# Kernel tuning notes

Hardware: AMD Instinct MI355X
Metric: run time of the kernel (lower is better)

Reference implementation:

```python
import jax, jax.numpy as jnp
import numpy as np

B, NR, NP, E, F, EIN, H, OUT = 2, 16384, 65536, 262144, 128, 4, 16, 4
EPS = 1e-6

def _mlp(x, W1, b1, W2, b2):
    return jax.nn.swish(x @ W1 + b1) @ W2 + b2

def _cond_norm(x, tau, C1, c1, C2, c2):
    # conditioned LayerNorm: scale/shift computed from tau by a shallow MLP
    h = jax.nn.swish(tau @ C1 + c1)               # [B, H]
    scale, shift = jnp.split(h @ C2 + c2, 2, -1)  # [B, F] each
    mu = jnp.mean(x, -1, keepdims=True)
    var = jnp.var(x, -1, keepdims=True)
    xn = (x - mu) * jax.lax.rsqrt(var + EPS)
    return xn * (1.0 + scale[:, None, :]) + shift[:, None, :]

def _segment_mean(feat, recv, num_segments):
    seg = lambda f, r: jax.ops.segment_sum(f, r, num_segments=num_segments)
    s = jax.vmap(seg)(feat, recv)
    cnt = jax.vmap(seg)(jnp.ones(recv.shape, feat.dtype), recv)
    return s / jnp.maximum(cnt, 1.0)[..., None]

def setup_inputs():
    key = jax.random.key(0)
    ks = iter(jax.random.split(key, 48))
    dense = lambda i, o: jax.random.normal(next(ks), (i, o), jnp.float32) / np.sqrt(i)
    inp = {}
    inp['rnode_features'] = jax.random.normal(next(ks), (B, NR, F), jnp.float32)
    inp['pnode_features'] = jax.random.normal(next(ks), (B, NP, F), jnp.float32)
    inp['edge_features'] = jax.random.normal(next(ks), (B, E, EIN), jnp.float32)
    inp['tau'] = jax.random.uniform(next(ks), (B, 1), jnp.float32)
    # edge embedding MLP + cond norm
    inp['We1'], inp['We2'] = dense(EIN, F), dense(F, F)
    inp['be1'], inp['be2'] = jnp.zeros((F,)), jnp.zeros((F,))
    inp['Ce1'], inp['Ce2'] = dense(1, H), dense(H, 2 * F)
    inp['ce1'], inp['ce2'] = jnp.zeros((H,)), jnp.zeros((2 * F,))
    # edge update MLP + cond norm
    inp['Wu1'], inp['Wu2'] = dense(3 * F, F), dense(F, F)
    inp['bu1'], inp['bu2'] = jnp.zeros((F,)), jnp.zeros((F,))
    inp['Cu1'], inp['Cu2'] = dense(1, H), dense(H, 2 * F)
    inp['cu1'], inp['cu2'] = jnp.zeros((H,)), jnp.zeros((2 * F,))
    # pnode update MLP + cond norm
    inp['Wp1'], inp['Wp2'] = dense(2 * F, F), dense(F, F)
    inp['bp1'], inp['bp2'] = jnp.zeros((F,)), jnp.zeros((F,))
    inp['Cp1'], inp['Cp2'] = dense(1, H), dense(H, 2 * F)
    inp['cp1'], inp['cp2'] = jnp.zeros((H,)), jnp.zeros((2 * F,))
    # rnode update MLP + cond norm
    inp['Wr1'], inp['Wr2'] = dense(F, F), dense(F, F)
    inp['br1'], inp['br2'] = jnp.zeros((F,)), jnp.zeros((F,))
    inp['Cr1'], inp['Cr2'] = dense(1, H), dense(H, 2 * F)
    inp['cr1'], inp['cr2'] = jnp.zeros((H,)), jnp.zeros((2 * F,))
    # pnode output MLP (no norm)
    inp['Wo1'], inp['Wo2'] = dense(F, F), dense(F, OUT)
    inp['bo1'], inp['bo2'] = jnp.zeros((F,)), jnp.zeros((OUT,))
    inp['senders'] = jax.random.randint(next(ks), (B, E), 0, NR, jnp.int32)
    inp['receivers'] = jax.random.randint(next(ks), (B, E), 0, NP, jnp.int32)
    return inp

def reference(rnode_features, pnode_features, edge_features, tau,
              We1, be1, We2, be2, Ce1, ce1, Ce2, ce2,
              Wu1, bu1, Wu2, bu2, Cu1, cu1, Cu2, cu2,
              Wp1, bp1, Wp2, bp2, Cp1, cp1, Cp2, cp2,
              Wr1, br1, Wr2, br2, Cr1, cr1, Cr2, cr2,
              Wo1, bo1, Wo2, bo2, senders, receivers):
    # 1) embed raw r2p edge features to latent size (embed_edges=True)
    e = _cond_norm(_mlp(edge_features, We1, be1, We2, be2), tau, Ce1, ce1, Ce2, ce2)
    # 2) one message-passing step: edge update from gathered sender/receiver feats
    sf = jnp.take_along_axis(rnode_features, senders[..., None], axis=1)    # [B,E,F]
    rf = jnp.take_along_axis(pnode_features, receivers[..., None], axis=1)  # [B,E,F]
    e = e + _cond_norm(_mlp(jnp.concatenate([e, sf, rf], -1), Wu1, bu1, Wu2, bu2),
                       tau, Cu1, cu1, Cu2, cu2)
    # 3) pnode update with segment_mean aggregation, residual
    agg = _segment_mean(e, receivers, NP)                                   # [B,NP,F]
    p = pnode_features + _cond_norm(
        _mlp(jnp.concatenate([pnode_features, agg], -1), Wp1, bp1, Wp2, bp2),
        tau, Cp1, cp1, Cp2, cp2)
    # 4) rnode update (no incoming edges; structurally present but unused by output)
    r = rnode_features + _cond_norm(_mlp(rnode_features, Wr1, br1, Wr2, br2),
                                    tau, Cr1, cr1, Cr2, cr2)
    del r
    # 5) output MLP on pnodes (node_output_size=dict(pnodes=num_outputs))
    return _mlp(p, Wo1, bo1, Wo2, bo2)
```

## Files before the change

### kernel.cpp

```cpp
#include <hip/hip_runtime.h>

constexpr int cB  = 2;
constexpr int cNR = 16384;
constexpr int cNP = 65536;
constexpr int cE  = 262144;
constexpr int cF  = 128;
constexpr int cEB = cE / 64;
constexpr int SP  = 136;
constexpr int EFP = 40;

typedef unsigned short u16;
using f32x4 = __attribute__((ext_vector_type(4))) float;
using s8v   = __attribute__((ext_vector_type(8))) short;

constexpr int G8_We2 = 0, G8_Wu1 = 16, G8_Wu2 = 64, G8_Wp1 = 80, G8_Wp2 = 112, G8_Wo1 = 128;
constexpr int G8_TOT = 144;
constexpr int SWZ_N = G8_TOT * 128 + 256 + 512;
constexpr int WB_WE1 = (G8_TOT * 128 + 256) * 8;

constexpr size_t WS_CNT  = 0;
constexpr size_t WS_POS  = WS_CNT + (size_t)cB * cNP;
constexpr size_t WS_BSUM = WS_POS + (size_t)cB * cNP;
constexpr size_t WS_SS   = WS_BSUM + 512;
constexpr size_t WS_WB   = WS_SS + 3 * cB * 256;
constexpr size_t WS_RB   = WS_WB + (size_t)SWZ_N * 4;
constexpr size_t WS_PB   = WS_RB + (size_t)cB * cNR * cF / 2;
constexpr size_t WS_EL   = WS_PB + (size_t)cB * cNP * cF / 2;
constexpr size_t WS_EB   = WS_EL + (size_t)cB * cE;

__device__ __forceinline__ float bf2f(u16 u) {
  union { unsigned int i; float f; } v; v.i = ((unsigned int)u) << 16; return v.f;
}
__device__ __forceinline__ u16 f2bf(float f) {
  union { float f; unsigned int i; } v; v.f = f;
  unsigned int x = v.i;
  return (u16)((x + 0x7fffu + ((x >> 16) & 1u)) >> 16);
}
__device__ __forceinline__ u16 f2bf_fast(float f) {
  return (u16)((__float_as_uint(f) + 0x8000u) >> 16);
}
__device__ __forceinline__ unsigned pack2(float a, float b) {
  return __builtin_amdgcn_perm(__float_as_uint(b) + 0x8000u,
                               __float_as_uint(a) + 0x8000u, 0x07060302u);
}
__device__ __forceinline__ float swishf(float x) {
  return x * __builtin_amdgcn_rcpf(1.0f + __expf(-x));
}

template <int CTRL>
__device__ __forceinline__ float dpp_add(float x) {
  int xi = __float_as_int(x);
  int r = __builtin_amdgcn_update_dpp(xi, xi, CTRL, 0xf, 0xf, false);
  return x + __int_as_float(r);
}

__device__ __forceinline__ void gload4_lds(const u16* gsrc, u16* lds) {
  __builtin_amdgcn_global_load_lds(
      (const __attribute__((address_space(1))) void*)gsrc,
      (__attribute__((address_space(3))) void*)lds, 4, 0, 0);
}

__device__ __forceinline__ void kloop128s(const u16* act, const u16* __restrict__ wbg,
                                          f32x4 (&acc)[4][2], int cw, int l16, int quad) {
  s8v bf[4][2];
#pragma unroll
  for (int k0 = 0; k0 < 4; ++k0)
#pragma unroll
    for (int ci = 0; ci < 2; ++ci)
      bf[k0][ci] = *(const s8v*)(wbg + ((size_t)(k0 * 4 + quad) * 128 + cw + ci * 16 + l16) * 8);
#pragma unroll
  for (int k0 = 0; k0 < 4; ++k0) {
    s8v af[4];
#pragma unroll
    for (int ri = 0; ri < 4; ++ri)
      af[ri] = *(const s8v*)(act + (size_t)(ri * 16 + l16) * SP + k0 * 32 + quad * 8);
#pragma unroll
    for (int ri = 0; ri < 4; ++ri)
#pragma unroll
      for (int ci = 0; ci < 2; ++ci)
        acc[ri][ci] = __builtin_amdgcn_mfma_f32_16x16x32_bf16(af[ri], bf[k0][ci], acc[ri][ci], 0, 0, 0);
  }
}

__device__ __forceinline__ void init_acc_s(f32x4 (&acc)[4][2], const float* __restrict__ bias,
                                           int cw, int l16) {
#pragma unroll
  for (int ci = 0; ci < 2; ++ci) {
    float bv = bias[cw + ci * 16 + l16];
#pragma unroll
    for (int ri = 0; ri < 4; ++ri) acc[ri][ci] = (f32x4){bv, bv, bv, bv};
  }
}

__device__ __forceinline__ void cond_norm_s(f32x4 (&acc)[4][2], float* red, float* musig,
                                            const float* __restrict__ ssp,
                                            int cw, int l16, int quad, int wv, int t) {
  __syncthreads();
#pragma unroll
  for (int ri = 0; ri < 4; ++ri)
#pragma unroll
    for (int reg = 0; reg < 4; ++reg) {
      float v0 = acc[ri][0][reg], v1 = acc[ri][1][reg];
      float s = v0 + v1;
      float q = v0 * v0 + v1 * v1;
      s = dpp_add<0x128>(s); q = dpp_add<0x128>(q);
      s = dpp_add<0x124>(s); q = dpp_add<0x124>(q);
      s = dpp_add<0x122>(s); q = dpp_add<0x122>(q);
      s = dpp_add<0x121>(s); q = dpp_add<0x121>(q);
      if (l16 == 0) {
        int row = ri * 16 + quad * 4 + reg;
        red[row * 8 + wv * 2]     = s;
        red[row * 8 + wv * 2 + 1] = q;
      }
    }
  __syncthreads();
  if (t < 64) {
    float sum = red[t * 8 + 0] + red[t * 8 + 2] + red[t * 8 + 4] + red[t * 8 + 6];
    float sq  = red[t * 8 + 1] + red[t * 8 + 3] + red[t * 8 + 5] + red[t * 8 + 7];
    float mu  = sum * (1.0f / 128.0f);
    float var = fmaxf(sq * (1.0f / 128.0f) - mu * mu, 0.0f);
    musig[t * 2]     = mu;
    musig[t * 2 + 1] = __builtin_amdgcn_rsqf(var + 1e-6f);
  }
  __syncthreads();
  float scl[2], shf[2];
#pragma unroll
  for (int ci = 0; ci < 2; ++ci) {
    int col = cw + ci * 16 + l16;
    scl[ci] = 1.0f + ssp[col];
    shf[ci] = ssp[128 + col];
  }
#pragma unroll
  for (int ri = 0; ri < 4; ++ri)
#pragma unroll
    for (int reg = 0; reg < 4; ++reg) {
      int row = ri * 16 + quad * 4 + reg;
      float mu = musig[row * 2], is = musig[row * 2 + 1];
#pragma unroll
      for (int ci = 0; ci < 2; ++ci)
        acc[ri][ci][reg] = (acc[ri][ci][reg] - mu) * is * scl[ci] + shf[ci];
    }
}

template <bool DOSWISH>
__device__ __forceinline__ void store_s(u16* buf, const f32x4 (&acc)[4][2],
                                        int cw, int l16, int quad) {
#pragma unroll
  for (int ri = 0; ri < 4; ++ri)
#pragma unroll
    for (int reg = 0; reg < 4; ++reg) {
      int row = ri * 16 + quad * 4 + reg;
#pragma unroll
      for (int ci = 0; ci < 2; ++ci) {
        float v = acc[ri][ci][reg];
        if (DOSWISH) v = swishf(v);
        buf[(size_t)row * SP + cw + ci * 16 + l16] = f2bf_fast(v);
      }
    }
}

__global__ void zero_kernel(float4* __restrict__ p, int n4) {
  int i = blockIdx.x * 256 + threadIdx.x;
  if (i < n4) p[i] = make_float4(0.f, 0.f, 0.f, 0.f);
}

__global__ void cvtn_kernel(const float* __restrict__ src, u16* __restrict__ dst, int n2) {
  int i = blockIdx.x * 256 + threadIdx.x;
  if (i >= n2) return;
  float2 v = ((const float2*)src)[i];
  ((unsigned*)dst)[i] = pack2(v.x, v.y);
}

__global__ void hist_kernel(const int* __restrict__ receivers, int* __restrict__ cntI) {
  int i = blockIdx.x * 256 + threadIdx.x;
  if (i >= cB * cE) return;
  int b = i / cE;
  int r = min(max(receivers[i], 0), cNP - 1);
  atomicAdd(&cntI[(size_t)b * cNP + r], 1);
}

__global__ void scanA_kernel(const int* __restrict__ cntI, int* __restrict__ bsum) {
  __shared__ int red[256];
  int g = blockIdx.x, t = threadIdx.x;
  red[t] = cntI[g * 256 + t];
  __syncthreads();
  for (int s = 128; s > 0; s >>= 1) {
    if (t < s) red[t] += red[t + s];
    __syncthreads();
  }
  if (t == 0) bsum[g] = red[0];
}

__global__ void scanB_kernel(int* __restrict__ bsum) {
  __shared__ int s0[512], s1[512];
  int t = threadIdx.x;
  int v0 = bsum[t];
  s0[t] = v0;
  __syncthreads();
  int* src = s0; int* dst = s1;
  for (int s = 1; s < 512; s <<= 1) {
    dst[t] = src[t] + ((t >= s) ? src[t - s] : 0);
    __syncthreads();
    int* tmp = src; src = dst; dst = tmp;
  }
  bsum[t] = src[t] - v0;
}

__global__ void scanC_kernel(const int* __restrict__ cntI, const int* __restrict__ bsum,
                             int* __restrict__ pos) {
  __shared__ int s0[256], s1[256];
  int g = blockIdx.x, t = threadIdx.x;
  int v0 = cntI[g * 256 + t];
  s0[t] = v0;
  __syncthreads();
  int* src = s0; int* dst = s1;
  for (int s = 1; s < 256; s <<= 1) {
    dst[t] = src[t] + ((t >= s) ? src[t - s] : 0);
    __syncthreads();
    int* tmp = src; src = dst; dst = tmp;
  }
  pos[g * 256 + t] = src[t] - v0 + bsum[g];
}

__global__ void fill_kernel(const int* __restrict__ receivers, int* __restrict__ pos,
                            int* __restrict__ elist) {
  int i = blockIdx.x * 256 + threadIdx.x;
  if (i >= cB * cE) return;
  int b = i / cE, e = i - b * cE;
  int r = min(max(receivers[i], 0), cNP - 1);
  int idx = atomicAdd(&pos[(size_t)b * cNP + r], 1);
  elist[idx] = e;
}

struct SwzSrc { const float* p[7]; };

__global__ void swz_kernel(SwzSrc s, const float* __restrict__ Wo2, u16* __restrict__ wb) {
  int t = blockIdx.x * 256 + threadIdx.x;
  if (t >= SWZ_N) return;
  if (t >= G8_TOT * 128 + 256) {
    int idx3 = t - (G8_TOT * 128 + 256);
    int k8 = idx3 >> 7, n = idx3 & 127;
    const float* We1 = s.p[6];
    u16 v[8];
#pragma unroll
    for (int j = 0; j < 8; ++j) {
      int k = k8 * 8 + j;
      v[j] = (k < 4) ? f2bf(We1[(size_t)k * 128 + n]) : (u16)0;
    }
    ((uint4*)wb)[t] = *(uint4*)v;
    return;
  }
  if (t >= G8_TOT * 128) {
    int idx2 = t - G8_TOT * 128;
    int k8 = idx2 >> 4, n = idx2 & 15;
    u16 v[8];
#pragma unroll
    for (int j = 0; j < 8; ++j)
      v[j] = (n < 4) ? f2bf(Wo2[(size_t)(k8 * 8 + j) * 4 + n]) : (u16)0;
    ((uint4*)wb)[G8_TOT * 128 + k8 * 16 + n] = *(uint4*)v;
    return;
  }
  int n = t & 127, g8 = t >> 7;
  int seg, base;
  if (g8 < G8_Wu1)      { seg = 0; base = G8_We2; }
  else if (g8 < G8_Wu2) { seg = 1; base = G8_Wu1; }
  else if (g8 < G8_Wp1) { seg = 2; base = G8_Wu2; }
  else if (g8 < G8_Wp2) { seg = 3; base = G8_Wp1; }
  else if (g8 < G8_Wo1) { seg = 4; base = G8_Wp2; }
  else                  { seg = 5; base = G8_Wo1; }
  const float* W = s.p[seg];
  int k8l = g8 - base;
  u16 v[8];
#pragma unroll
  for (int j = 0; j < 8; ++j) v[j] = f2bf(W[(size_t)(k8l * 8 + j) * 128 + n]);
  ((uint4*)wb)[g8 * 128 + n] = *(uint4*)v;
}

__global__ void cond_kernel(const float* __restrict__ tau,
                            const float* __restrict__ Ce1, const float* __restrict__ ce1,
                            const float* __restrict__ Ce2, const float* __restrict__ ce2,
                            const float* __restrict__ Cu1, const float* __restrict__ cu1,
                            const float* __restrict__ Cu2, const float* __restrict__ cu2,
                            const float* __restrict__ Cp1, const float* __restrict__ cp1,
                            const float* __restrict__ Cp2, const float* __restrict__ cp2,
                            float* __restrict__ ss) {
  int set = blockIdx.x, b = blockIdx.y, j = threadIdx.x;
  const float *C1, *c1, *C2, *c2;
  if (set == 0)      { C1 = Ce1; c1 = ce1; C2 = Ce2; c2 = ce2; }
  else if (set == 1) { C1 = Cu1; c1 = cu1; C2 = Cu2; c2 = cu2; }
  else               { C1 = Cp1; c1 = cp1; C2 = Cp2; c2 = cp2; }
  float tf = tau[b];
  float a = c2[j];
  for (int k = 0; k < 16; ++k) {
    float h = swishf(tf * C1[k] + c1[k]);
    a = fmaf(h, C2[k * 256 + j], a);
  }
  ss[(size_t)set * cB * 256 + (size_t)b * 256 + j] = a;
}

struct EWb { const float *be1, *be2, *bu1, *bu2; };

struct __align__(16) EdgeSmem {
  u16 bufE[64 * SP];
  u16 bufX[64 * SP];
  union {
    u16 ef[64 * EFP];
    struct { float red[512]; float musig[128]; } r;
  } u;
  int sidx[64], ridx[64];
};

__global__ __launch_bounds__(256, 4) void edge_mfma(
    const u16* __restrict__ rnb, const u16* __restrict__ pnb,
    const float* __restrict__ efeat, const int* __restrict__ senders,
    const int* __restrict__ receivers, const int* __restrict__ elist,
    EWb w, const u16* __restrict__ wb,
    const float* __restrict__ ss, u16* __restrict__ ebuf) {
  __shared__ EdgeSmem sm;
  const int t = threadIdx.x, wv = t >> 6, lane = t & 63, l16 = lane & 15, quad = lane >> 4;
  const int cw = wv * 32;
  const int raw = blockIdx.x;
  const int swz = (raw & 7) * (cB * cEB / 8) + (raw >> 3);
  const int b   = swz / cEB;

  if (t < 64) {
    int eid = elist[(size_t)swz * 64 + t];
    size_t ge = (size_t)b * cE + eid;
    sm.sidx[t] = min(max(senders[ge], 0), cNR - 1);
    sm.ridx[t] = min(max(receivers[ge], 0), cNP - 1);
    float4 ef = *(const float4*)(efeat + ge * 4);
    uint4 w0 = { pack2(ef.x, ef.y), pack2(ef.z, ef.w), 0u, 0u };
    uint4 zz = { 0u, 0u, 0u, 0u };
    uint4* rowp = (uint4*)(sm.u.ef + (size_t)t * EFP);
    rowp[0] = w0; rowp[1] = zz; rowp[2] = zz; rowp[3] = zz; rowp[4] = zz;
  }
  __syncthreads();

  f32x4 acc[4][2];

  init_acc_s(acc, w.be1, cw, l16);
  {
    const u16* wbe1 = wb + WB_WE1;
    s8v bf0 = *(const s8v*)(wbe1 + ((size_t)quad * 128 + cw + l16) * 8);
    s8v bf1 = *(const s8v*)(wbe1 + ((size_t)quad * 128 + cw + 16 + l16) * 8);
#pragma unroll
    for (int ri = 0; ri < 4; ++ri) {
      s8v af = *(const s8v*)(sm.u.ef + (size_t)(ri * 16 + l16) * EFP + quad * 8);
      acc[ri][0] = __builtin_amdgcn_mfma_f32_16x16x32_bf16(af, bf0, acc[ri][0], 0, 0, 0);
      acc[ri][1] = __builtin_amdgcn_mfma_f32_16x16x32_bf16(af, bf1, acc[ri][1], 0, 0, 0);
    }
  }
  store_s<true>(sm.bufX, acc, cw, l16, quad);
  __syncthreads();

  init_acc_s(acc, w.be2, cw, l16);
  kloop128s(sm.bufX, wb + (size_t)G8_We2 * 1024, acc, cw, l16, quad);
  cond_norm_s(acc, sm.u.r.red, sm.u.r.musig, ss + (size_t)b * 256, cw, l16, quad, wv, t);
  store_s<false>(sm.bufE, acc, cw, l16, quad);

#pragma unroll
  for (int rr = 0; rr < 16; ++rr) {
    int row = wv * 16 + rr;
    gload4_lds(rnb + ((size_t)b * cNR + sm.sidx[row]) * cF + lane * 2,
               sm.bufX + (size_t)row * SP);
  }
  f32x4 accU[4][2];
  init_acc_s(accU, w.bu1, cw, l16);
  __syncthreads();
  kloop128s(sm.bufX, wb + (size_t)(G8_Wu1 + 16) * 1024, accU, cw, l16, quad);
  __syncthreads();
#pragma unroll
  for (int rr = 0; rr < 16; ++rr) {
    int row = wv * 16 + rr;
    gload4_lds(pnb + ((size_t)b * cNP + sm.ridx[row]) * cF + lane * 2,
               sm.bufX + (size_t)row * SP);
  }
  kloop128s(sm.bufE, wb + (size_t)G8_Wu1 * 1024, accU, cw, l16, quad);
  __syncthreads();
  kloop128s(sm.bufX, wb + (size_t)(G8_Wu1 + 32) * 1024, accU, cw, l16, quad);
  __syncthreads();
  store_s<true>(sm.bufX, accU, cw, l16, quad);
  __syncthreads();

  init_acc_s(acc, w.bu2, cw, l16);
  kloop128s(sm.bufX, wb + (size_t)G8_Wu2 * 1024, acc, cw, l16, quad);
  cond_norm_s(acc, sm.u.r.red, sm.u.r.musig, ss + (size_t)(cB + b) * 256, cw, l16, quad, wv, t);

#pragma unroll
  for (int ri = 0; ri < 4; ++ri)
#pragma unroll
    for (int reg = 0; reg < 4; ++reg) {
      int row = ri * 16 + quad * 4 + reg;
#pragma unroll
      for (int ci = 0; ci < 2; ++ci)
        acc[ri][ci][reg] += bf2f(sm.bufE[(size_t)row * SP + cw + ci * 16 + l16]);
    }
  store_s<false>(sm.bufX, acc, cw, l16, quad);
  __syncthreads();
#pragma unroll
  for (int rr = 0; rr < 16; ++rr) {
    int row = wv * 16 + rr;
    unsigned v = *(const unsigned*)(sm.bufX + (size_t)row * SP + lane * 2);
    ((unsigned*)ebuf)[((size_t)(swz * 64 + row)) * 64 + lane] = v;
  }
}

struct PWb { const float *bp1, *bp2, *bo1, *bo2; };

struct __align__(16) PnodeSmem {
  u16 bufP[64 * SP];
  u16 bufX[64 * SP];
  float red[512];
  float musig[128];
  float cinv[64];
  int startA[64];
  int endA[72];
};

__global__ __launch_bounds__(256, 4) void pnode_mfma(
    const u16* __restrict__ pnb, PWb w, const u16* __restrict__ wb,
    const float* __restrict__ ss, const unsigned* __restrict__ eb32,
    const int* __restrict__ cntI, const int* __restrict__ pos,
    float* __restrict__ out) {
  __shared__ PnodeSmem sm;
  const int t = threadIdx.x, wv = t >> 6, lane = t & 63, l16 = lane & 15, quad = lane >> 4;
  const int cw = wv * 32;
  const int b  = blockIdx.y;
  const int n0 = blockIdx.x * 64;

  if (t < 64) {
    size_t g = (size_t)b * cNP + n0 + t;
    int c  = cntI[g];
    int e_ = pos[g];
    sm.startA[t] = e_ - c;
    sm.endA[t]   = e_;
    sm.cinv[t]   = __builtin_amdgcn_rcpf(fmaxf((float)c, 1.0f));
  } else if (t < 72) {
    sm.endA[t] = 0x7fffffff;
  }
  __syncthreads();

#pragma unroll
  for (int rr = 0; rr < 16; ++rr) {
    int row = wv * 16 + rr;
    unsigned pvu = *(const unsigned*)(pnb + (((size_t)b * cNP + n0 + row) * cF + lane * 2));
    *(unsigned*)(sm.bufP + (size_t)row * SP + lane * 2) = pvu;
  }

  {
    const int nodeLo = wv * 16;
    int cur  = nodeLo;
    int bnd  = sm.endA[cur];
    int s    = sm.startA[nodeLo];
    const int sEnd = sm.endA[nodeLo + 15];
    float a0 = 0.f, a1 = 0.f;
    for (; s < sEnd; s += 8) {
      unsigned v[8];
      int m = sEnd - s;
#pragma unroll
      for (int j = 0; j < 8; ++j)
        if (j < m) v[j] = eb32[(size_t)(s + j) * 64 + lane];
#pragma unroll
      for (int j = 0; j < 8; ++j) {
        if (j < m) {
          while (s + j == bnd) {
            float ci = sm.cinv[cur];
            *(unsigned*)(sm.bufX + (size_t)cur * SP + lane * 2) = pack2(a0 * ci, a1 * ci);
            a0 = a1 = 0.f; ++cur; bnd = sm.endA[cur];
          }
          a0 += bf2f((u16)(v[j] & 0xffffu));
          a1 += bf2f((u16)(v[j] >> 16));
        }
      }
    }
    while (cur < nodeLo + 16) {
      float ci = sm.cinv[cur];
      *(unsigned*)(sm.bufX + (size_t)cur * SP + lane * 2) = pack2(a0 * ci, a1 * ci);
      a0 = a1 = 0.f; ++cur;
    }
  }
  __syncthreads();

  f32x4 acc[4][2];

  init_acc_s(acc, w.bp1, cw, l16);
  kloop128s(sm.bufP, wb + (size_t)G8_Wp1 * 1024, acc, cw, l16, quad);
  kloop128s(sm.bufX, wb + (size_t)(G8_Wp1 + 16) * 1024, acc, cw, l16, quad);
  __syncthreads();
  store_s<true>(sm.bufX, acc, cw, l16, quad);
  __syncthreads();

  init_acc_s(acc, w.bp2, cw, l16);
  kloop128s(sm.bufX, wb + (size_t)G8_Wp2 * 1024, acc, cw, l16, quad);
  cond_norm_s(acc, sm.red, sm.musig, ss + (size_t)(2 * cB + b) * 256, cw, l16, quad, wv, t);
#pragma unroll
  for (int ri = 0; ri < 4; ++ri)
#pragma unroll
    for (int reg = 0; reg < 4; ++reg) {
      int row = ri * 16 + quad * 4 + reg;
#pragma unroll
      for (int ci = 0; ci < 2; ++ci)
        acc[ri][ci][reg] += bf2f(sm.bufP[(size_t)row * SP + cw + ci * 16 + l16]);
    }
  __syncthreads();
  store_s<false>(sm.bufP, acc, cw, l16, quad);
  __syncthreads();

  init_acc_s(acc, w.bo1, cw, l16);
  kloop128s(sm.bufP, wb + (size_t)G8_Wo1 * 1024, acc, cw, l16, quad);
  store_s<true>(sm.bufX, acc, cw, l16, quad);
  __syncthreads();

  {
    const u16* wo2 = wb + (size_t)G8_TOT * 1024;
    float bv = (l16 < 4) ? w.bo2[l16] : 0.0f;
    f32x4 a1 = {bv, bv, bv, bv};
#pragma unroll
    for (int k0 = 0; k0 < 4; ++k0) {
      s8v af = *(const s8v*)(sm.bufX + (size_t)(wv * 16 + l16) * SP + k0 * 32 + quad * 8);
      s8v bf = *(const s8v*)(wo2 + ((size_t)(k0 * 4 + quad) * 16 + l16) * 8);
      a1 = __builtin_amdgcn_mfma_f32_16x16x32_bf16(af, bf, a1, 0, 0, 0);
    }
    if (l16 < 4) {
      size_t obase = (size_t)b * cNP + n0 + wv * 16 + quad * 4;
#pragma unroll
      for (int reg = 0; reg < 4; ++reg)
        out[(obase + reg) * 4 + l16] = a1[reg];
    }
  }
}

extern "C" void kernel_launch(void* const* d_in, const int* in_sizes, int n_in,
                              void* d_out, int out_size, void* d_ws, size_t ws_size,
                              hipStream_t stream) {
  const float* rnode = (const float*)d_in[0];
  const float* pnode = (const float*)d_in[1];
  const float* efeat = (const float*)d_in[2];
  const float* tau   = (const float*)d_in[3];
  const int* senders   = (const int*)d_in[40];
  const int* receivers = (const int*)d_in[41];
  float* ws = (float*)d_ws;
  int* cntI  = (int*)(ws + WS_CNT);
  int* pos   = (int*)(ws + WS_POS);
  int* bsum  = (int*)(ws + WS_BSUM);
  u16* wb    = (u16*)(ws + WS_WB);
  u16* rnb   = (u16*)(ws + WS_RB);
  u16* pnb   = (u16*)(ws + WS_PB);
  int* elist = (int*)(ws + WS_EL);
  u16* ebuf  = (u16*)(ws + WS_EB);

  SwzSrc sw;
  sw.p[0] = (const float*)d_in[5];
  sw.p[1] = (const float*)d_in[12];
  sw.p[2] = (const float*)d_in[13];
  sw.p[3] = (const float*)d_in[20];
  sw.p[4] = (const float*)d_in[21];
  sw.p[5] = (const float*)d_in[36];
  sw.p[6] = (const float*)d_in[4];
  swz_kernel<<<(SWZ_N + 255) / 256, 256, 0, stream>>>(sw, (const float*)d_in[37], wb);

  const int nrn2 = (int)((size_t)cB * cNR * cF / 2);
  cvtn_kernel<<<(nrn2 + 255) / 256, 256, 0, stream>>>(rnode, rnb, nrn2);
  const int npn2 = (int)((size_t)cB * cNP * cF / 2);
  cvtn_kernel<<<(npn2 + 255) / 256, 256, 0, stream>>>(pnode, pnb, npn2);

  cond_kernel<<<dim3(3, cB), 256, 0, stream>>>(
      tau,
      (const float*)d_in[8],  (const float*)d_in[10],
      (const float*)d_in[9],  (const float*)d_in[11],
      (const float*)d_in[16], (const float*)d_in[18],
      (const float*)d_in[17], (const float*)d_in[19],
      (const float*)d_in[24], (const float*)d_in[26],
      (const float*)d_in[25], (const float*)d_in[27],
      ws + WS_SS);

  const int n4 = (int)((size_t)cB * cNP * 4 / 16);
  zero_kernel<<<(n4 + 255) / 256, 256, 0, stream>>>((float4*)cntI, n4);
  const int nBE = cB * cE;
  hist_kernel<<<(nBE + 255) / 256, 256, 0, stream>>>(receivers, cntI);
  scanA_kernel<<<512, 256, 0, stream>>>(cntI, bsum);
  scanB_kernel<<<1, 512, 0, stream>>>(bsum);
  scanC_kernel<<<512, 256, 0, stream>>>(cntI, bsum, pos);
  fill_kernel<<<(nBE + 255) / 256, 256, 0, stream>>>(receivers, pos, elist);

  EWb ew = { (const float*)d_in[6], (const float*)d_in[7],
             (const float*)d_in[14], (const float*)d_in[15] };
  PWb pw = { (const float*)d_in[22], (const float*)d_in[23], (const float*)d_in[38],
             (const float*)d_in[39] };

  edge_mfma<<<dim3(cB * cEB), 256, 0, stream>>>(
      rnb, pnb, efeat, senders, receivers, elist, ew, wb,
      ws + WS_SS, ebuf);

  pnode_mfma<<<dim3(cNP / 64, cB), 256, 0, stream>>>(
      pnb, pw, wb, ws + WS_SS, (const unsigned*)ebuf, cntI, pos,
      (float*)d_out);
}
```

Measured before the change: 468.9 us.

## Store edge output directly from registers with permuted Wp1 rows, fuse conversions

The edge kernel now packs the residual-added edge features straight from MFMA accumulators into the global edge buffer in a column-permuted order. This removes an LDS staging store, a barrier and a reread. The Wp1 weight rows for the aggregated half are permuted in the swizzle kernel to match the new layout, which the later segment-mean aggregation relies on. The two bf16 conversion launches are merged into one, and uniform LDS indices are hoisted to scalars with readfirstlane. 32-bit LDS index arithmetic replaces size_t. The risk is that the permutation must line up exactly with the pnode kernel's accumulation order, and the direct global stores are less coalesced.

```diff
diff --git a/kernel.cpp b/kernel.cpp
--- a/kernel.cpp
+++ b/kernel.cpp
@@ -73,7 +73,7 @@
     s8v af[4];
 #pragma unroll
     for (int ri = 0; ri < 4; ++ri)
-      af[ri] = *(const s8v*)(act + (size_t)(ri * 16 + l16) * SP + k0 * 32 + quad * 8);
+      af[ri] = *(const s8v*)(act + (ri * 16 + l16) * SP + k0 * 32 + quad * 8);
 #pragma unroll
     for (int ri = 0; ri < 4; ++ri)
 #pragma unroll
@@ -154,7 +154,7 @@
       for (int ci = 0; ci < 2; ++ci) {
         float v = acc[ri][ci][reg];
         if (DOSWISH) v = swishf(v);
-        buf[(size_t)row * SP + cw + ci * 16 + l16] = f2bf_fast(v);
+        buf[row * SP + cw + ci * 16 + l16] = f2bf_fast(v);
       }
     }
 }
@@ -164,11 +164,17 @@
   if (i < n4) p[i] = make_float4(0.f, 0.f, 0.f, 0.f);
 }
 
-__global__ void cvtn_kernel(const float* __restrict__ src, u16* __restrict__ dst, int n2) {
+__global__ void cvtn2_kernel(const float* __restrict__ sa, u16* __restrict__ da, int n2a,
+                             const float* __restrict__ sb, u16* __restrict__ db, int n2b) {
   int i = blockIdx.x * 256 + threadIdx.x;
-  if (i >= n2) return;
-  float2 v = ((const float2*)src)[i];
-  ((unsigned*)dst)[i] = pack2(v.x, v.y);
+  if (i < n2a) {
+    float2 v = ((const float2*)sa)[i];
+    ((unsigned*)da)[i] = pack2(v.x, v.y);
+  } else if (i < n2a + n2b) {
+    int k = i - n2a;
+    float2 v = ((const float2*)sb)[k];
+    ((unsigned*)db)[k] = pack2(v.x, v.y);
+  }
 }
 
 __global__ void hist_kernel(const int* __restrict__ receivers, int* __restrict__ cntI) {
@@ -272,7 +278,15 @@
   int k8l = g8 - base;
   u16 v[8];
 #pragma unroll
-  for (int j = 0; j < 8; ++j) v[j] = f2bf(W[(size_t)(k8l * 8 + j) * 128 + n]);
+  for (int j = 0; j < 8; ++j) {
+    int kd = k8l * 8 + j;
+    int ks = kd;
+    if (seg == 3 && kd >= 128) {
+      int p = kd - 128;
+      ks = 128 + ((p >> 5) << 5) + ((p & 1) << 4) + ((p & 31) >> 1);
+    }
+    v[j] = f2bf(W[(size_t)ks * 128 + n]);
+  }
   ((uint4*)wb)[g8 * 128 + n] = *(uint4*)v;
 }
 
@@ -345,7 +359,7 @@
     s8v bf1 = *(const s8v*)(wbe1 + ((size_t)quad * 128 + cw + 16 + l16) * 8);
 #pragma unroll
     for (int ri = 0; ri < 4; ++ri) {
-      s8v af = *(const s8v*)(sm.u.ef + (size_t)(ri * 16 + l16) * EFP + quad * 8);
+      s8v af = *(const s8v*)(sm.u.ef + (ri * 16 + l16) * EFP + quad * 8);
       acc[ri][0] = __builtin_amdgcn_mfma_f32_16x16x32_bf16(af, bf0, acc[ri][0], 0, 0, 0);
       acc[ri][1] = __builtin_amdgcn_mfma_f32_16x16x32_bf16(af, bf1, acc[ri][1], 0, 0, 0);
     }
@@ -361,8 +375,9 @@
 #pragma unroll
   for (int rr = 0; rr < 16; ++rr) {
     int row = wv * 16 + rr;
-    gload4_lds(rnb + ((size_t)b * cNR + sm.sidx[row]) * cF + lane * 2,
-               sm.bufX + (size_t)row * SP);
+    int si = __builtin_amdgcn_readfirstlane(sm.sidx[row]);
+    gload4_lds(rnb + ((size_t)b * cNR + si) * cF + lane * 2,
+               sm.bufX + row * SP);
   }
   f32x4 accU[4][2];
   init_acc_s(accU, w.bu1, cw, l16);
@@ -372,8 +387,9 @@
 #pragma unroll
   for (int rr = 0; rr < 16; ++rr) {
     int row = wv * 16 + rr;
-    gload4_lds(pnb + ((size_t)b * cNP + sm.ridx[row]) * cF + lane * 2,
-               sm.bufX + (size_t)row * SP);
+    int ri_ = __builtin_amdgcn_readfirstlane(sm.ridx[row]);
+    gload4_lds(pnb + ((size_t)b * cNP + ri_) * cF + lane * 2,
+               sm.bufX + row * SP);
   }
   kloop128s(sm.bufE, wb + (size_t)G8_Wu1 * 1024, accU, cw, l16, quad);
   __syncthreads();
@@ -386,22 +402,17 @@
   kloop128s(sm.bufX, wb + (size_t)G8_Wu2 * 1024, acc, cw, l16, quad);
   cond_norm_s(acc, sm.u.r.red, sm.u.r.musig, ss + (size_t)(cB + b) * 256, cw, l16, quad, wv, t);
 
-#pragma unroll
-  for (int ri = 0; ri < 4; ++ri)
-#pragma unroll
-    for (int reg = 0; reg < 4; ++reg) {
-      int row = ri * 16 + quad * 4 + reg;
-#pragma unroll
-      for (int ci = 0; ci < 2; ++ci)
-        acc[ri][ci][reg] += bf2f(sm.bufE[(size_t)row * SP + cw + ci * 16 + l16]);
-    }
-  store_s<false>(sm.bufX, acc, cw, l16, quad);
-  __syncthreads();
-#pragma unroll
-  for (int rr = 0; rr < 16; ++rr) {
-    int row = wv * 16 + rr;
-    unsigned v = *(const unsigned*)(sm.bufX + (size_t)row * SP + lane * 2);
-    ((unsigned*)ebuf)[((size_t)(swz * 64 + row)) * 64 + lane] = v;
+  {
+    unsigned* eb32o = (unsigned*)ebuf + (size_t)(swz * 64) * 64;
+#pragma unroll
+    for (int ri = 0; ri < 4; ++ri)
+#pragma unroll
+      for (int reg = 0; reg < 4; ++reg) {
+        int row = ri * 16 + quad * 4 + reg;
+        float v0 = acc[ri][0][reg] + bf2f(sm.bufE[row * SP + cw + l16]);
+        float v1 = acc[ri][1][reg] + bf2f(sm.bufE[row * SP + cw + 16 + l16]);
+        eb32o[(size_t)row * 64 + wv * 16 + l16] = pack2(v0, v1);
+      }
   }
 }
 
@@ -444,15 +455,15 @@
   for (int rr = 0; rr < 16; ++rr) {
     int row = wv * 16 + rr;
     unsigned pvu = *(const unsigned*)(pnb + (((size_t)b * cNP + n0 + row) * cF + lane * 2));
-    *(unsigned*)(sm.bufP + (size_t)row * SP + lane * 2) = pvu;
+    *(unsigned*)(sm.bufP + row * SP + lane * 2) = pvu;
   }
 
   {
     const int nodeLo = wv * 16;
     int cur  = nodeLo;
-    int bnd  = sm.endA[cur];
-    int s    = sm.startA[nodeLo];
-    const int sEnd = sm.endA[nodeLo + 15];
+    int bnd  = __builtin_amdgcn_readfirstlane(sm.endA[cur]);
+    int s    = __builtin_amdgcn_readfirstlane(sm.startA[nodeLo]);
+    const int sEnd = __builtin_amdgcn_readfirstlane(sm.endA[nodeLo + 15]);
     float a0 = 0.f, a1 = 0.f;
     for (; s < sEnd; s += 8) {
       unsigned v[8];
@@ -465,8 +476,9 @@
         if (j < m) {
           while (s + j == bnd) {
             float ci = sm.cinv[cur];
-            *(unsigned*)(sm.bufX + (size_t)cur * SP + lane * 2) = pack2(a0 * ci, a1 * ci);
-            a0 = a1 = 0.f; ++cur; bnd = sm.endA[cur];
+            *(unsigned*)(sm.bufX + cur * SP + lane * 2) = pack2(a0 * ci, a1 * ci);
+            a0 = a1 = 0.f; ++cur;
+            bnd = __builtin_amdgcn_readfirstlane(sm.endA[cur]);
           }
           a0 += bf2f((u16)(v[j] & 0xffffu));
           a1 += bf2f((u16)(v[j] >> 16));
@@ -475,7 +487,7 @@
     }
     while (cur < nodeLo + 16) {
       float ci = sm.cinv[cur];
-      *(unsigned*)(sm.bufX + (size_t)cur * SP + lane * 2) = pack2(a0 * ci, a1 * ci);
+      *(unsigned*)(sm.bufX + cur * SP + lane * 2) = pack2(a0 * ci, a1 * ci);
       a0 = a1 = 0.f; ++cur;
     }
   }
@@ -500,7 +512,7 @@
       int row = ri * 16 + quad * 4 + reg;
 #pragma unroll
       for (int ci = 0; ci < 2; ++ci)
-        acc[ri][ci][reg] += bf2f(sm.bufP[(size_t)row * SP + cw + ci * 16 + l16]);
+        acc[ri][ci][reg] += bf2f(sm.bufP[row * SP + cw + ci * 16 + l16]);
     }
   __syncthreads();
   store_s<false>(sm.bufP, acc, cw, l16, quad);
@@ -517,7 +529,7 @@
     f32x4 a1 = {bv, bv, bv, bv};
 #pragma unroll
     for (int k0 = 0; k0 < 4; ++k0) {
-      s8v af = *(const s8v*)(sm.bufX + (size_t)(wv * 16 + l16) * SP + k0 * 32 + quad * 8);
+      s8v af = *(const s8v*)(sm.bufX + (wv * 16 + l16) * SP + k0 * 32 + quad * 8);
       s8v bf = *(const s8v*)(wo2 + ((size_t)(k0 * 4 + quad) * 16 + l16) * 8);
       a1 = __builtin_amdgcn_mfma_f32_16x16x32_bf16(af, bf, a1, 0, 0, 0);
     }
@@ -560,9 +572,9 @@
   swz_kernel<<<(SWZ_N + 255) / 256, 256, 0, stream>>>(sw, (const float*)d_in[37], wb);
 
   const int nrn2 = (int)((size_t)cB * cNR * cF / 2);
-  cvtn_kernel<<<(nrn2 + 255) / 256, 256, 0, stream>>>(rnode, rnb, nrn2);
   const int npn2 = (int)((size_t)cB * cNP * cF / 2);
-  cvtn_kernel<<<(npn2 + 255) / 256, 256, 0, stream>>>(pnode, pnb, npn2);
+  cvtn2_kernel<<<(nrn2 + npn2 + 255) / 256, 256, 0, stream>>>(
+      rnode, rnb, nrn2, pnode, pnb, npn2);
 
   cond_kernel<<<dim3(3, cB), 256, 0, stream>>>(
       tau,
```

Result: faster. 456.4 us (-2.7%).
